# Kernel tuning notes

Hardware: AMD Instinct MI355X
Metric: run time of the kernel (lower is better)

## Reference

```python
import jax, jax.numpy as jnp
import numpy as np

GRID = 7  # kernel hard-codes 7x7 spatial grid
NEG = -1.0e20


def setup_inputs() -> dict:
    key = jax.random.key(0)
    ks = jax.random.split(key, 6)
    N, Cq, Cv = 512, 64, 512
    B = N * GRID
    return {
        "qH": jax.random.normal(ks[0], (B, GRID, Cq), dtype=jnp.float32),
        "kH": jax.random.normal(ks[1], (B, Cq, GRID), dtype=jnp.float32),
        "vH": jax.random.normal(ks[2], (B, Cv, GRID), dtype=jnp.float32),
        "qW": jax.random.normal(ks[3], (B, GRID, Cq), dtype=jnp.float32),
        "kW": jax.random.normal(ks[4], (B, Cq, GRID), dtype=jnp.float32),
        "vW": jax.random.normal(ks[5], (B, Cv, GRID), dtype=jnp.float32),
        "N": N,
    }


def reference(qH, kH, vH, qW, kW, vW, N):
    # H-direction tensors are folded as batch index bw = n*7 + w; attend over h-axis.
    # W-direction tensors are folded as batch index bh = n*7 + h; attend over w-axis.
    Cq = qH.shape[-1]
    Cv = vH.shape[1]
    qHr = qH.reshape(N, GRID, GRID, Cq)   # [n, w, h, c]
    kHr = kH.reshape(N, GRID, Cq, GRID)   # [n, w, c, j]
    vHr = vH.reshape(N, GRID, Cv, GRID)   # [n, w, c, j]
    qWr = qW.reshape(N, GRID, GRID, Cq)   # [n, h, w, c]
    kWr = kW.reshape(N, GRID, Cq, GRID)   # [n, h, c, y]
    vWr = vW.reshape(N, GRID, Cv, GRID)   # [n, h, c, y]

    # Column (H-axis) logits, with self-position (j == h) masked to -1e20.
    eH = jnp.einsum("nwhc,nwcj->nwhj", qHr, kHr)          # [n, w, h, j]
    eye = jnp.eye(GRID, dtype=bool)[None, None]            # mask on (h, j)
    eH = jnp.where(eye, jnp.float32(NEG), eH)
    # Row (W-axis) logits, no mask.
    eW = jnp.einsum("nhwc,nhcy->nhwy", qWr, kWr)          # [n, h, w, y]

    # Fused softmax over the 14 concatenated H+W logits per (n, h, w).
    logits = jnp.concatenate([eH.transpose(0, 2, 1, 3), eW], axis=-1)  # [n, h, w, 14]
    p = jax.nn.softmax(logits, axis=-1)
    pH = p[..., :GRID].transpose(0, 2, 1, 3)               # [n, w, h, j]
    pW = p[..., GRID:]                                     # [n, h, w, y]

    outH = jnp.einsum("nwhj,nwcj->nchw", pH, vHr)
    outW = jnp.einsum("nhwy,nhcy->nchw", pW, vWr)
    return outH + outW                                     # [n, Cv, 7, 7]
```

## Files before the change

### kernel.cpp

```cpp
#include <hip/hip_runtime.h>


#define NEGINF (-1e20f)

constexpr int QK_SLICE = 7 * 7 * 64;
constexpr int V_SLICE  = 7 * 512 * 7;

__device__ __forceinline__ void g2l4(const float* g, float* l) {
    __builtin_amdgcn_global_load_lds(
        (const __attribute__((address_space(1))) void*)g,
        (__attribute__((address_space(3))) void*)l, 4, 0, 0);
}

__global__ __launch_bounds__(512, 4) void fused_axial(
    const float* __restrict__ qH, const float* __restrict__ kH,
    const float* __restrict__ vH, const float* __restrict__ qW,
    const float* __restrict__ kW, const float* __restrict__ vW,
    float* __restrict__ out)
{
    __shared__ float sm[13937];
    float* A0 = sm;
    float* B0 = sm + 3164;
    float* U1 = sm + 6328;
    float* P  = sm + 13104;

    const int n    = blockIdx.x;
    const int t    = threadIdx.x;
    const int lane = t & 63;
    const int wv   = t >> 6;

    const float* qHn = qH + n * QK_SLICE;
    const float* kHn = kH + n * QK_SLICE;
    const float* qWn = qW + n * QK_SLICE;
    const float* kWn = kW + n * QK_SLICE;
    const float* vHn = vH + n * V_SLICE;
    const float* vWn = vW + n * V_SLICE;
    float* outn = out + n * V_SLICE;

    #pragma unroll
    for (int u = 0; u < 13; ++u) {
        const int r = wv + 8 * u;
        if (u < 12 || r < 98) {
            const int arr = r >= 49;
            const int wj  = r - 49 * arr;
            const int a   = (wj * 37) >> 8;
            const int j   = wj - 7 * a;
            const float* src = (arr ? kWn : kHn) + a * 448 + lane * 7 + j;
            float* dst = U1 + arr * 3388 + a * 484 + j * 68;
            g2l4(src, dst);
        }
    }
    __syncthreads();

    {
        const int b = lane >> 3;
        const int j = lane & 7;
        auto logit_group = [&](int gi) {
            const int arr = gi >= 7;
            const int a   = gi - 7 * arr;
            if (b < 7 && j < 7) {
                const float* qrow = (arr ? qWn : qHn) + (a * 7 + b) * 64;
                const float* krow = U1 + arr * 3388 + a * 484 + j * 68;
                float e = 0.f;
                #pragma unroll
                for (int cc = 0; cc < 64; cc += 4) {
                    float4 qv = *(const float4*)(qrow + cc);
                    float4 kv = *(const float4*)(krow + cc);
                    e += qv.x * kv.x + qv.y * kv.y + qv.z * kv.z + qv.w * kv.w;
                }
                if (!arr) {
                    if (b == j) e = NEGINF;
                    P[(b * 7 + a) * 17 + j] = e;
                } else {
                    P[(a * 7 + b) * 17 + 7 + j] = e;
                }
            }
        };
        logit_group(wv);
        if (wv < 6) logit_group(wv + 8);
    }
    __syncthreads();

    auto issue_v = [&](float* dstb, const float* srcb, int c0) {
        const float* s0 = srcb + c0 * 7 + lane;
        #pragma unroll
        for (int u = 0; u < 7; ++u) {
            const int r = wv + 8 * u;
            if (u < 6 || r < 49) {
                const int w2   = (r * 37) >> 8;
                const int part = r - 7 * w2;
                g2l4(s0 + w2 * 3584 + part * 64, dstb + w2 * 452 + part * 64);
            }
        }
    };

    issue_v(A0,        vHn, 0);
    issue_v(B0,        vWn, 0);
    issue_v(U1,        vHn, 64);
    issue_v(U1 + 3164, vWn, 64);

    if (t < 49) {
        float* row = P + t * 17;
        float l[14];
        float m = -3.4e38f;
        #pragma unroll
        for (int k = 0; k < 14; ++k) { l[k] = row[k]; m = fmaxf(m, l[k]); }
        float s = 0.f;
        #pragma unroll
        for (int k = 0; k < 14; ++k) { l[k] = __expf(l[k] - m); s += l[k]; }
        float inv = 1.f / s;
        #pragma unroll
        for (int k = 0; k < 14; ++k) row[k] = l[k] * inv;
    }
    __syncthreads();

    const int g  = (t * 1339) >> 16;
    const int hw = t - g * 49;
    const int h  = (hw * 37) >> 8;
    const int w  = hw - 7 * h;
    const bool active = (t < 490);

    float pr[14];
    if (active) {
        #pragma unroll
        for (int k = 0; k < 14; ++k) pr[k] = P[hw * 17 + k];
    }

    for (int chunk = 0; chunk < 8; ++chunk) {
        float* As = (chunk & 1) ? U1        : A0;
        float* Bs = (chunk & 1) ? U1 + 3164 : B0;
        const int c0 = chunk * 64;

        if (active) {
            const float* rowA = As + w * 452;
            const float* rowB = Bs + h * 452;
            #pragma unroll
            for (int it = 0; it < 2; ++it) {
                if (it == 0 || g < 6) {
                    const int quad = g + 10 * it;
                    const float* ra = rowA + quad * 28;
                    const float* rb = rowB + quad * 28;
                    float ac[4] = {0.f, 0.f, 0.f, 0.f};
                    #pragma unroll
                    for (int q = 0; q < 7; ++q) {
                        float4 f = *(const float4*)(ra + 4 * q);
                        ac[(4 * q + 0) / 7] += pr[(4 * q + 0) % 7] * f.x;
                        ac[(4 * q + 1) / 7] += pr[(4 * q + 1) % 7] * f.y;
                        ac[(4 * q + 2) / 7] += pr[(4 * q + 2) % 7] * f.z;
                        ac[(4 * q + 3) / 7] += pr[(4 * q + 3) % 7] * f.w;
                    }
                    #pragma unroll
                    for (int q = 0; q < 7; ++q) {
                        float4 f = *(const float4*)(rb + 4 * q);
                        ac[(4 * q + 0) / 7] += pr[7 + (4 * q + 0) % 7] * f.x;
                        ac[(4 * q + 1) / 7] += pr[7 + (4 * q + 1) % 7] * f.y;
                        ac[(4 * q + 2) / 7] += pr[7 + (4 * q + 2) % 7] * f.z;
                        ac[(4 * q + 3) / 7] += pr[7 + (4 * q + 3) % 7] * f.w;
                    }
                    float* o = outn + (c0 + quad * 4) * 49 + hw;
                    o[0]   = ac[0];
                    o[49]  = ac[1];
                    o[98]  = ac[2];
                    o[147] = ac[3];
                }
            }
        }
        __syncthreads();
        if (chunk < 6) {
            issue_v(As, vHn, (chunk + 2) * 64);
            issue_v(Bs, vWn, (chunk + 2) * 64);
        }
    }
}

extern "C" void kernel_launch(void* const* d_in, const int* in_sizes, int n_in,
                              void* d_out, int out_size, void* d_ws, size_t ws_size,
                              hipStream_t stream) {
    const float* qH = (const float*)d_in[0];
    const float* kH = (const float*)d_in[1];
    const float* vH = (const float*)d_in[2];
    const float* qW = (const float*)d_in[3];
    const float* kW = (const float*)d_in[4];
    const float* vW = (const float*)d_in[5];
    float* out = (float*)d_out;
    fused_axial<<<512, 512, 0, stream>>>(qH, kH, vH, qW, kW, vW, out);
}
```

Measured before the change: 178.5 us.

## Split each sample across four channel-quarter blocks with XCD-aware block swizzle

The kernel now launches four blocks per sample, each covering 128 of the 512 value channels, instead of one block per sample. Each block recomputes the 98-logit softmax for its sample. The block-to-work mapping is swizzled so that the four blocks of one sample land on the same XCD and can share K/Q reads through L2. Shared memory is shrunk to a double-buffered set of 32-channel V tiles, with the next tile's prefetch issued before the current compute, and the launch bound is raised to allow more resident blocks. The aim is to fill the GPU better than 512 blocks can; the cost is four times the Q/K loads and logit work, plus fewer active threads per block.

```diff
diff --git a/kernel.cpp b/kernel.cpp
--- a/kernel.cpp
+++ b/kernel.cpp
@@ -12,19 +12,21 @@
         (__attribute__((address_space(3))) void*)l, 4, 0, 0);
 }
 
-__global__ __launch_bounds__(512, 4) void fused_axial(
+__global__ __launch_bounds__(512, 8) void fused_axial(
     const float* __restrict__ qH, const float* __restrict__ kH,
     const float* __restrict__ vH, const float* __restrict__ qW,
     const float* __restrict__ kW, const float* __restrict__ vW,
     float* __restrict__ out)
 {
-    __shared__ float sm[13937];
-    float* A0 = sm;
-    float* B0 = sm + 3164;
-    float* U1 = sm + 6328;
-    float* P  = sm + 13104;
+    __shared__ float sm[7609];
+    float* R = sm;
+    float* P = sm + 6776;
 
-    const int n    = blockIdx.x;
+    const int bid  = blockIdx.x;
+    const int work = (bid & 7) * 256 + (bid >> 3);
+    const int n    = work >> 2;
+    const int cq   = work & 3;
+    const int c0base = cq * 128;
     const int t    = threadIdx.x;
     const int lane = t & 63;
     const int wv   = t >> 6;
@@ -46,7 +48,7 @@
             const int a   = (wj * 37) >> 8;
             const int j   = wj - 7 * a;
             const float* src = (arr ? kWn : kHn) + a * 448 + lane * 7 + j;
-            float* dst = U1 + arr * 3388 + a * 484 + j * 68;
+            float* dst = R + arr * 3388 + a * 484 + j * 68;
             g2l4(src, dst);
         }
     }
@@ -60,7 +62,7 @@
             const int a   = gi - 7 * arr;
             if (b < 7 && j < 7) {
                 const float* qrow = (arr ? qWn : qHn) + (a * 7 + b) * 64;
-                const float* krow = U1 + arr * 3388 + a * 484 + j * 68;
+                const float* krow = R + arr * 3388 + a * 484 + j * 68;
                 float e = 0.f;
                 #pragma unroll
                 for (int cc = 0; cc < 64; cc += 4) {
@@ -84,20 +86,23 @@
     auto issue_v = [&](float* dstb, const float* srcb, int c0) {
         const float* s0 = srcb + c0 * 7 + lane;
         #pragma unroll
-        for (int u = 0; u < 7; ++u) {
+        for (int u = 0; u < 4; ++u) {
             const int r = wv + 8 * u;
-            if (u < 6 || r < 49) {
-                const int w2   = (r * 37) >> 8;
-                const int part = r - 7 * w2;
-                g2l4(s0 + w2 * 3584 + part * 64, dstb + w2 * 452 + part * 64);
+            if (r < 28 && ((r & 3) < 3 || lane < 32)) {
+                const int w2   = r >> 2;
+                const int part = r & 3;
+                g2l4(s0 + w2 * 3584 + part * 64, dstb + w2 * 228 + part * 64);
             }
         }
     };
 
-    issue_v(A0,        vHn, 0);
-    issue_v(B0,        vWn, 0);
-    issue_v(U1,        vHn, 64);
-    issue_v(U1 + 3164, vWn, 64);
+    float* S0A = R;
+    float* S0B = R + 1596;
+    float* S1A = R + 3192;
+    float* S1B = R + 4788;
+
+    issue_v(S0A, vHn, c0base);
+    issue_v(S0B, vWn, c0base);
 
     if (t < 49) {
         float* row = P + t * 17;
@@ -118,7 +123,7 @@
     const int hw = t - g * 49;
     const int h  = (hw * 37) >> 8;
     const int w  = hw - 7 * h;
-    const bool active = (t < 490);
+    const bool active = (t < 392);
 
     float pr[14];
     if (active) {
@@ -126,50 +131,44 @@
         for (int k = 0; k < 14; ++k) pr[k] = P[hw * 17 + k];
     }
 
-    for (int chunk = 0; chunk < 8; ++chunk) {
-        float* As = (chunk & 1) ? U1        : A0;
-        float* Bs = (chunk & 1) ? U1 + 3164 : B0;
-        const int c0 = chunk * 64;
+    for (int chunk = 0; chunk < 4; ++chunk) {
+        float* As = (chunk & 1) ? S1A : S0A;
+        float* Bs = (chunk & 1) ? S1B : S0B;
+
+        if (chunk < 3) {
+            float* nA = (chunk & 1) ? S0A : S1A;
+            float* nB = (chunk & 1) ? S0B : S1B;
+            issue_v(nA, vHn, c0base + (chunk + 1) * 32);
+            issue_v(nB, vWn, c0base + (chunk + 1) * 32);
+        }
 
         if (active) {
-            const float* rowA = As + w * 452;
-            const float* rowB = Bs + h * 452;
+            const float* rowA = As + w * 228 + g * 28;
+            const float* rowB = Bs + h * 228 + g * 28;
+            float ac[4] = {0.f, 0.f, 0.f, 0.f};
             #pragma unroll
-            for (int it = 0; it < 2; ++it) {
-                if (it == 0 || g < 6) {
-                    const int quad = g + 10 * it;
-                    const float* ra = rowA + quad * 28;
-                    const float* rb = rowB + quad * 28;
-                    float ac[4] = {0.f, 0.f, 0.f, 0.f};
-                    #pragma unroll
-                    for (int q = 0; q < 7; ++q) {
-                        float4 f = *(const float4*)(ra + 4 * q);
-                        ac[(4 * q + 0) / 7] += pr[(4 * q + 0) % 7] * f.x;
-                        ac[(4 * q + 1) / 7] += pr[(4 * q + 1) % 7] * f.y;
-                        ac[(4 * q + 2) / 7] += pr[(4 * q + 2) % 7] * f.z;
-                        ac[(4 * q + 3) / 7] += pr[(4 * q + 3) % 7] * f.w;
-                    }
-                    #pragma unroll
-                    for (int q = 0; q < 7; ++q) {
-                        float4 f = *(const float4*)(rb + 4 * q);
-                        ac[(4 * q + 0) / 7] += pr[7 + (4 * q + 0) % 7] * f.x;
-                        ac[(4 * q + 1) / 7] += pr[7 + (4 * q + 1) % 7] * f.y;
-                        ac[(4 * q + 2) / 7] += pr[7 + (4 * q + 2) % 7] * f.z;
-                        ac[(4 * q + 3) / 7] += pr[7 + (4 * q + 3) % 7] * f.w;
-                    }
-                    float* o = outn + (c0 + quad * 4) * 49 + hw;
-                    o[0]   = ac[0];
-                    o[49]  = ac[1];
-                    o[98]  = ac[2];
-                    o[147] = ac[3];
-                }
+            for (int q = 0; q < 7; ++q) {
+                float4 f = *(const float4*)(rowA + 4 * q);
+                ac[(4 * q + 0) / 7] += pr[(4 * q + 0) % 7] * f.x;
+                ac[(4 * q + 1) / 7] += pr[(4 * q + 1) % 7] * f.y;
+                ac[(4 * q + 2) / 7] += pr[(4 * q + 2) % 7] * f.z;
+                ac[(4 * q + 3) / 7] += pr[(4 * q + 3) % 7] * f.w;
             }
+            #pragma unroll
+            for (int q = 0; q < 7; ++q) {
+                float4 f = *(const float4*)(rowB + 4 * q);
+                ac[(4 * q + 0) / 7] += pr[7 + (4 * q + 0) % 7] * f.x;
+                ac[(4 * q + 1) / 7] += pr[7 + (4 * q + 1) % 7] * f.y;
+                ac[(4 * q + 2) / 7] += pr[7 + (4 * q + 2) % 7] * f.z;
+                ac[(4 * q + 3) / 7] += pr[7 + (4 * q + 3) % 7] * f.w;
+            }
+            float* o = outn + (c0base + chunk * 32 + g * 4) * 49 + hw;
+            o[0]   = ac[0];
+            o[49]  = ac[1];
+            o[98]  = ac[2];
+            o[147] = ac[3];
         }
-        __syncthreads();
-        if (chunk < 6) {
-            issue_v(As, vHn, (chunk + 2) * 64);
-            issue_v(Bs, vWn, (chunk + 2) * 64);
-        }
+        if (chunk < 3) __syncthreads();
     }
 }
 
@@ -183,5 +182,5 @@
     const float* kW = (const float*)d_in[4];
     const float* vW = (const float*)d_in[5];
     float* out = (float*)d_out;
-    fused_axial<<<512, 512, 0, stream>>>(qH, kH, vH, qW, kW, vW, out);
+    fused_axial<<<2048, 512, 0, stream>>>(qH, kH, vH, qW, kW, vW, out);
 }
```

Result: slower. 187.8 us (+5.2%).

## Replace syncthreads with fine-grained vmcnt waits and issue V chunk 0 earlier

Applied to the files above, without the earlier changes.

Issues the first V chunk loads alongside the K loads before the logit phase. It replaces __syncthreads with explicit s_waitcnt vmcnt/lgkmcnt counters plus raw s_barrier, so each barrier only waits for the oldest outstanding global-to-LDS loads rather than draining every in-flight transfer. This lets the double-buffered V prefetch actually overlap with compute. The risk is that an incorrect vmcnt count (12, which must match the per-thread number of issued loads) could cause a race, and the extra barriers per chunk add some sync overhead.

```diff
diff --git a/kernel.cpp b/kernel.cpp
--- a/kernel.cpp
+++ b/kernel.cpp
@@ -11,6 +11,19 @@
         (const __attribute__((address_space(1))) void*)g,
         (__attribute__((address_space(3))) void*)l, 4, 0, 0);
 }
+__device__ __forceinline__ void waitv12() {
+    asm volatile("s_waitcnt vmcnt(12)" ::: "memory");
+    __builtin_amdgcn_sched_barrier(0);
+}
+__device__ __forceinline__ void waitv0() {
+    asm volatile("s_waitcnt vmcnt(0)" ::: "memory");
+    __builtin_amdgcn_sched_barrier(0);
+}
+__device__ __forceinline__ void waitlgkm0() {
+    asm volatile("s_waitcnt lgkmcnt(0)" ::: "memory");
+    __builtin_amdgcn_sched_barrier(0);
+}
+__device__ __forceinline__ void bar() { __builtin_amdgcn_s_barrier(); }
 
 __global__ __launch_bounds__(512, 4) void fused_axial(
     const float* __restrict__ qH, const float* __restrict__ kH,
@@ -22,6 +35,8 @@
     float* A0 = sm;
     float* B0 = sm + 3164;
     float* U1 = sm + 6328;
+    float* A1 = U1;
+    float* B1 = U1 + 3164;
     float* P  = sm + 13104;
 
     const int n    = blockIdx.x;
@@ -36,6 +51,19 @@
     const float* vHn = vH + n * V_SLICE;
     const float* vWn = vW + n * V_SLICE;
     float* outn = out + n * V_SLICE;
+
+    auto issue_v = [&](float* dstb, const float* srcb, int c0) {
+        const float* s0 = srcb + c0 * 7 + lane;
+        #pragma unroll
+        for (int u = 0; u < 7; ++u) {
+            const int r = wv + 8 * u;
+            if (u < 6 || r < 49) {
+                const int w2   = (r * 37) >> 8;
+                const int part = r - 7 * w2;
+                g2l4(s0 + w2 * 3584 + part * 64, dstb + w2 * 452 + part * 64);
+            }
+        }
+    };
 
     #pragma unroll
     for (int u = 0; u < 13; ++u) {
@@ -50,7 +78,10 @@
             g2l4(src, dst);
         }
     }
-    __syncthreads();
+    issue_v(A0, vHn, 0);
+    issue_v(B0, vWn, 0);
+    waitv12();
+    bar();
 
     {
         const int b = lane >> 3;
@@ -79,25 +110,11 @@
         logit_group(wv);
         if (wv < 6) logit_group(wv + 8);
     }
-    __syncthreads();
-
-    auto issue_v = [&](float* dstb, const float* srcb, int c0) {
-        const float* s0 = srcb + c0 * 7 + lane;
-        #pragma unroll
-        for (int u = 0; u < 7; ++u) {
-            const int r = wv + 8 * u;
-            if (u < 6 || r < 49) {
-                const int w2   = (r * 37) >> 8;
-                const int part = r - 7 * w2;
-                g2l4(s0 + w2 * 3584 + part * 64, dstb + w2 * 452 + part * 64);
-            }
-        }
-    };
-
-    issue_v(A0,        vHn, 0);
-    issue_v(B0,        vWn, 0);
-    issue_v(U1,        vHn, 64);
-    issue_v(U1 + 3164, vWn, 64);
+    waitlgkm0();
+    bar();
+
+    issue_v(A1, vHn, 64);
+    issue_v(B1, vWn, 64);
 
     if (t < 49) {
         float* row = P + t * 17;
@@ -112,7 +129,9 @@
         #pragma unroll
         for (int k = 0; k < 14; ++k) row[k] = l[k] * inv;
     }
-    __syncthreads();
+    waitlgkm0();
+    waitv12();
+    bar();
 
     const int g  = (t * 1339) >> 16;
     const int hw = t - g * 49;
@@ -127,8 +146,8 @@
     }
 
     for (int chunk = 0; chunk < 8; ++chunk) {
-        float* As = (chunk & 1) ? U1        : A0;
-        float* Bs = (chunk & 1) ? U1 + 3164 : B0;
+        float* As = (chunk & 1) ? A1 : A0;
+        float* Bs = (chunk & 1) ? B1 : B0;
         const int c0 = chunk * 64;
 
         if (active) {
@@ -165,11 +184,17 @@
                 }
             }
         }
-        __syncthreads();
+        if (chunk == 7) break;
+        waitlgkm0();
+        bar();
         if (chunk < 6) {
             issue_v(As, vHn, (chunk + 2) * 64);
             issue_v(Bs, vWn, (chunk + 2) * 64);
-        }
+            waitv12();
+        } else {
+            waitv0();
+        }
+        bar();
     }
 }
 
```

Measured after the change: 177.9 us. No clear change (-0.3%).

## Read V directly from global memory instead of double-buffered LDS staging

Applied to the files above, without the earlier changes.

Removes the LDS double-buffer pipeline for the V tensors (async global-to-LDS loads plus a barrier per chunk). Each thread now reads its float4 V rows straight from global memory, relying on caches, because several threads share the same rows. LDS use drops from about 56KB to about 30KB, which could raise occupancy and removes the per-chunk syncs. In exchange it gives up explicit prefetch overlap and depends on L1/L2 hit rates for the repeated reads.

```diff
diff --git a/kernel.cpp b/kernel.cpp
--- a/kernel.cpp
+++ b/kernel.cpp
@@ -18,11 +18,9 @@
     const float* __restrict__ kW, const float* __restrict__ vW,
     float* __restrict__ out)
 {
-    __shared__ float sm[13937];
-    float* A0 = sm;
-    float* B0 = sm + 3164;
-    float* U1 = sm + 6328;
-    float* P  = sm + 13104;
+    __shared__ float sm[7609];
+    float* R = sm;
+    float* P = sm + 6776;
 
     const int n    = blockIdx.x;
     const int t    = threadIdx.x;
@@ -46,7 +44,7 @@
             const int a   = (wj * 37) >> 8;
             const int j   = wj - 7 * a;
             const float* src = (arr ? kWn : kHn) + a * 448 + lane * 7 + j;
-            float* dst = U1 + arr * 3388 + a * 484 + j * 68;
+            float* dst = R + arr * 3388 + a * 484 + j * 68;
             g2l4(src, dst);
         }
     }
@@ -60,7 +58,7 @@
             const int a   = gi - 7 * arr;
             if (b < 7 && j < 7) {
                 const float* qrow = (arr ? qWn : qHn) + (a * 7 + b) * 64;
-                const float* krow = U1 + arr * 3388 + a * 484 + j * 68;
+                const float* krow = R + arr * 3388 + a * 484 + j * 68;
                 float e = 0.f;
                 #pragma unroll
                 for (int cc = 0; cc < 64; cc += 4) {
@@ -81,24 +79,6 @@
     }
     __syncthreads();
 
-    auto issue_v = [&](float* dstb, const float* srcb, int c0) {
-        const float* s0 = srcb + c0 * 7 + lane;
-        #pragma unroll
-        for (int u = 0; u < 7; ++u) {
-            const int r = wv + 8 * u;
-            if (u < 6 || r < 49) {
-                const int w2   = (r * 37) >> 8;
-                const int part = r - 7 * w2;
-                g2l4(s0 + w2 * 3584 + part * 64, dstb + w2 * 452 + part * 64);
-            }
-        }
-    };
-
-    issue_v(A0,        vHn, 0);
-    issue_v(B0,        vWn, 0);
-    issue_v(U1,        vHn, 64);
-    issue_v(U1 + 3164, vWn, 64);
-
     if (t < 49) {
         float* row = P + t * 17;
         float l[14];
@@ -118,28 +98,23 @@
     const int hw = t - g * 49;
     const int h  = (hw * 37) >> 8;
     const int w  = hw - 7 * h;
-    const bool active = (t < 490);
 
-    float pr[14];
-    if (active) {
+    if (t < 490) {
+        float pr[14];
         #pragma unroll
         for (int k = 0; k < 14; ++k) pr[k] = P[hw * 17 + k];
-    }
 
-    for (int chunk = 0; chunk < 8; ++chunk) {
-        float* As = (chunk & 1) ? U1        : A0;
-        float* Bs = (chunk & 1) ? U1 + 3164 : B0;
-        const int c0 = chunk * 64;
+        const float* baseA = vHn + w * 3584;
+        const float* baseB = vWn + h * 3584;
 
-        if (active) {
-            const float* rowA = As + w * 452;
-            const float* rowB = Bs + h * 452;
+        for (int chunk = 0; chunk < 8; ++chunk) {
             #pragma unroll
             for (int it = 0; it < 2; ++it) {
                 if (it == 0 || g < 6) {
                     const int quad = g + 10 * it;
-                    const float* ra = rowA + quad * 28;
-                    const float* rb = rowB + quad * 28;
+                    const int coff = (chunk * 64 + quad * 4) * 7;
+                    const float* ra = baseA + coff;
+                    const float* rb = baseB + coff;
                     float ac[4] = {0.f, 0.f, 0.f, 0.f};
                     #pragma unroll
                     for (int q = 0; q < 7; ++q) {
@@ -157,18 +132,13 @@
                         ac[(4 * q + 2) / 7] += pr[7 + (4 * q + 2) % 7] * f.z;
                         ac[(4 * q + 3) / 7] += pr[7 + (4 * q + 3) % 7] * f.w;
                     }
-                    float* o = outn + (c0 + quad * 4) * 49 + hw;
+                    float* o = outn + (chunk * 64 + quad * 4) * 49 + hw;
                     o[0]   = ac[0];
                     o[49]  = ac[1];
                     o[98]  = ac[2];
                     o[147] = ac[3];
                 }
             }
-        }
-        __syncthreads();
-        if (chunk < 6) {
-            issue_v(As, vHn, (chunk + 2) * 64);
-            issue_v(Bs, vWn, (chunk + 2) * 64);
         }
     }
 }
```

After: 200.9 us. 1.13x slower.
